# Optimization experiments

Measured on AMD Instinct MI355X. Metric: run time of the kernel, lower is better.

Reference implementation:

```python
import jax, jax.numpy as jnp
import numpy as np

N = 100000      # nodes
E = 1600000     # edges (before self loops)
IN_F = 128
OUT_F = 32
HEADS = 4
NEG_SLOPE = 0.2


def setup_inputs() -> dict:
    key = jax.random.key(0)
    k1, k2, k3, k4, k5, k6 = jax.random.split(key, 6)
    x = jax.random.normal(k1, (N, IN_F), dtype=jnp.float32)
    edge_index = jax.random.randint(k2, (2, E), 0, N, dtype=jnp.int64)
    # PyG GATConv params: shared linear W [in, H*F], attention vectors att_src/att_dst [1,H,F], bias [H*F]
    glorot = (6.0 / (IN_F + HEADS * OUT_F)) ** 0.5
    W = jax.random.uniform(k3, (IN_F, HEADS * OUT_F), dtype=jnp.float32, minval=-glorot, maxval=glorot)
    ga = (6.0 / (1 + OUT_F)) ** 0.5
    att_src = jax.random.uniform(k4, (HEADS, OUT_F), dtype=jnp.float32, minval=-ga, maxval=ga)
    att_dst = jax.random.uniform(k5, (HEADS, OUT_F), dtype=jnp.float32, minval=-ga, maxval=ga)
    bias = jnp.zeros((HEADS * OUT_F,), dtype=jnp.float32)
    return {"x": x, "edge_index": edge_index, "W": W, "att_src": att_src, "att_dst": att_dst, "bias": bias}


def reference(x, edge_index, W, att_src, att_dst, bias):
    n = x.shape[0]
    # add self loops (PyG add_self_loops=True)
    loops = jnp.arange(n, dtype=edge_index.dtype)
    src = jnp.concatenate([edge_index[0], loops])  # [E+N] message source j
    dst = jnp.concatenate([edge_index[1], loops])  # [E+N] message target i

    h = (x @ W).reshape(n, HEADS, OUT_F)                 # [N,H,F]
    a_src = jnp.sum(h * att_src[None], axis=-1)          # [N,H]
    a_dst = jnp.sum(h * att_dst[None], axis=-1)          # [N,H]

    e = a_src[src] + a_dst[dst]                          # [E',H]
    e = jax.nn.leaky_relu(e, NEG_SLOPE)
    # per-destination softmax over incoming edges
    m = jax.ops.segment_max(e, dst, num_segments=n)      # [N,H]
    ex = jnp.exp(e - m[dst])
    s = jax.ops.segment_sum(ex, dst, num_segments=n)     # [N,H]
    alpha = ex / (s[dst] + 1e-16)                        # [E',H]

    msg = h[src] * alpha[:, :, None]                     # [E',H,F]
    out = jax.ops.segment_sum(msg, dst, num_segments=n)  # [N,H,F]
    return out.reshape(n, HEADS * OUT_F) + bias
```

## Files before the change

### kernel.cpp

```cpp
#include <hip/hip_runtime.h>


#define NEG_SLOPE 0.2f
#define NB_MAX 256
#define BSHIFT 9
#define CHUNK 4096
#define CAP 11264

typedef __attribute__((ext_vector_type(8))) short short8;
typedef __attribute__((ext_vector_type(4))) float f32x4;

__device__ __forceinline__ unsigned int rne16(unsigned int u) {
  return (u + 0x7fffu + ((u >> 16) & 1u)) >> 16;
}
__device__ __forceinline__ unsigned int f2bf_pack(float a, float b) {
  return (rne16(__float_as_uint(b)) << 16) | (rne16(__float_as_uint(a)) & 0xffffu);
}

__global__ void k_wprep(const float* __restrict__ W, unsigned short* __restrict__ Wt) {
  int idx = blockIdx.x * 256 + threadIdx.x;
  int k = idx >> 7, col = idx & 127;
  Wt[col * 128 + k] = (unsigned short)rne16(__float_as_uint(W[idx]));
}

__global__ __launch_bounds__(256) void k_bucket_hist(
    const int* __restrict__ ei, int* __restrict__ bucketCnt, int E) {
  __shared__ int h[NB_MAX];
  int tid = threadIdx.x;
  h[tid] = 0;
  __syncthreads();
  int base = blockIdx.x * CHUNK;
  int n = E - base; if (n > CHUNK) n = CHUNK;
  for (int i = tid; i < n; i += 256) atomicAdd(&h[ei[E + base + i] >> BSHIFT], 1);
  __syncthreads();
  if (h[tid]) atomicAdd(&bucketCnt[tid], h[tid]);
}

__global__ void k_bucket_scan(const int* __restrict__ bucketCnt,
                              int* __restrict__ bucketOff, int* __restrict__ bcur) {
  int lane = threadIdx.x;
  int base = lane * 4;
  int v0 = bucketCnt[base], v1 = bucketCnt[base + 1];
  int v2 = bucketCnt[base + 2], v3 = bucketCnt[base + 3];
  int s = v0 + v1 + v2 + v3;
  int inc = s;
#pragma unroll
  for (int d = 1; d < 64; d <<= 1) {
    int t = __shfl_up(inc, d, 64);
    if (lane >= d) inc += t;
  }
  int ex = inc - s;
  bucketOff[base] = ex;          bcur[base] = ex;
  bucketOff[base + 1] = ex + v0; bcur[base + 1] = ex + v0;
  bucketOff[base + 2] = ex + v0 + v1; bcur[base + 2] = ex + v0 + v1;
  bucketOff[base + 3] = ex + v0 + v1 + v2; bcur[base + 3] = ex + v0 + v1 + v2;
  if (lane == 63) bucketOff[256] = inc;
}

__global__ __launch_bounds__(256) void k_bin(
    const int* __restrict__ ei, int* __restrict__ bcur,
    unsigned int* __restrict__ binned, int E, int nb) {
  __shared__ uint2 buf[CHUNK];
  __shared__ int hist[NB_MAX];
  __shared__ int loc[NB_MAX];
  __shared__ int gbase[NB_MAX];
  int tid = threadIdx.x;
  int e0 = blockIdx.x * CHUNK;
  int n = E - e0; if (n > CHUNK) n = CHUNK;

  for (int i = tid; i < NB_MAX; i += 256) hist[i] = 0;
  __syncthreads();

  int dstv[CHUNK / 256];
  int rankv[CHUNK / 256];
#pragma unroll
  for (int j = 0; j < CHUNK / 256; ++j) {
    int idx = j * 256 + tid;
    dstv[j] = -1;
    if (idx < n) {
      int d = ei[E + e0 + idx];
      dstv[j] = d;
      rankv[j] = atomicAdd(&hist[d >> BSHIFT], 1);
    }
  }
  __syncthreads();

  if (tid < 64) {
    int base = tid * 4;
    int v0 = hist[base], v1 = hist[base + 1], v2 = hist[base + 2], v3 = hist[base + 3];
    int s = v0 + v1 + v2 + v3;
    int inc = s;
#pragma unroll
    for (int d = 1; d < 64; d <<= 1) {
      int t = __shfl_up(inc, d, 64);
      if (tid >= d) inc += t;
    }
    int ex = inc - s;
    loc[base] = ex; loc[base + 1] = ex + v0;
    loc[base + 2] = ex + v0 + v1; loc[base + 3] = ex + v0 + v1 + v2;
  }
  __syncthreads();

#pragma unroll
  for (int j = 0; j < CHUNK / 256; ++j) {
    if (dstv[j] >= 0) {
      int s = ei[e0 + j * 256 + tid];
      int b = dstv[j] >> BSHIFT;
      buf[loc[b] + rankv[j]] = make_uint2((unsigned)s, (unsigned)dstv[j]);
    }
  }
  for (int b = tid; b < nb; b += 256)
    if (hist[b] > 0) gbase[b] = atomicAdd(&bcur[b], hist[b]);
  __syncthreads();

  for (int s = tid; s < n; s += 256) {
    uint2 p = buf[s];
    int b = (int)(p.y >> BSHIFT);
    binned[gbase[b] + (s - loc[b])] = p.x | ((p.y & 511u) << 20);
  }
}

__global__ __launch_bounds__(256) void k_scatter2(
    const unsigned int* __restrict__ binned, const int* __restrict__ bucketOff,
    int* __restrict__ off, int* __restrict__ ssrc, int Nn, int E, int nb) {
  __shared__ int cnt[512];
  __shared__ int loc[512];
  __shared__ int obuf[CAP];
  __shared__ int wsum[4];
  int b = blockIdx.x, tid = threadIdx.x;
  int node0 = b << BSHIFT;
  int nnodes = Nn - node0; if (nnodes > 512) nnodes = 512;
  int base = bucketOff[b];
  int nE = bucketOff[b + 1] - base;

  cnt[tid] = 0; cnt[tid + 256] = 0;
  __syncthreads();
  for (int i = tid; i < nE; i += 256)
    atomicAdd(&cnt[(binned[base + i] >> 20) & 511u], 1);
  __syncthreads();

  int i0 = 2 * tid, i1 = 2 * tid + 1;
  int v0 = cnt[i0] + (i0 < nnodes ? 1 : 0);
  int v1 = cnt[i1] + (i1 < nnodes ? 1 : 0);
  int s = v0 + v1;
  int lane = tid & 63, w = tid >> 6;
  int inc = s;
#pragma unroll
  for (int d = 1; d < 64; d <<= 1) {
    int t = __shfl_up(inc, d, 64);
    if (lane >= d) inc += t;
  }
  if (lane == 63) wsum[w] = inc;
  __syncthreads();
  int wbase = 0;
  for (int ww = 0; ww < w; ++ww) wbase += wsum[ww];
  int ex = wbase + inc - s;
  loc[i0] = ex; loc[i1] = ex + v0;
  __syncthreads();

  int csrBase = base + node0;
  for (int i = tid; i < nnodes; i += 256) {
    int l = loc[i];
    off[node0 + i] = csrBase + l;
    obuf[l] = node0 + i;
  }
  for (int i = tid; i < 512; i += 256) cnt[i] = loc[i] + 1;
  __syncthreads();

  for (int i = tid; i < nE; i += 256) {
    unsigned p = binned[base + i];
    int d = (p >> 20) & 511u;
    int pos = atomicAdd(&cnt[d], 1);
    if (pos < CAP) obuf[pos] = (int)(p & 0xFFFFFu);
  }
  __syncthreads();

  int tot = nE + nnodes;
  for (int i = tid; i < tot; i += 256) ssrc[csrBase + i] = obuf[i];
  if (b == nb - 1 && tid == 0) off[Nn] = E + Nn;
}

__global__ __launch_bounds__(256) void k_gemm(
    const float* __restrict__ x, const unsigned short* __restrict__ Wt,
    unsigned int* __restrict__ hb, int Nn) {
  int tid = threadIdx.x;
  int w = tid >> 6, lane = tid & 63;
  int m = lane & 15, q = lane >> 4;
  int r0 = blockIdx.x * 64 + w * 16;
  int rowA = r0 + m; if (rowA >= Nn) rowA = Nn - 1;
  const float* xrow = x + (size_t)rowA * 128;

  f32x4 acc[8];
#pragma unroll
  for (int t = 0; t < 8; ++t) acc[t] = (f32x4){0.f, 0.f, 0.f, 0.f};

#pragma unroll
  for (int ks = 0; ks < 4; ++ks) {
    int k0 = ks * 32 + q * 8;
    float4 a0 = *(const float4*)(xrow + k0);
    float4 a1 = *(const float4*)(xrow + k0 + 4);
    unsigned au[4];
    au[0] = f2bf_pack(a0.x, a0.y);
    au[1] = f2bf_pack(a0.z, a0.w);
    au[2] = f2bf_pack(a1.x, a1.y);
    au[3] = f2bf_pack(a1.z, a1.w);
    short8 af = *(short8*)au;
#pragma unroll
    for (int t = 0; t < 8; ++t) {
      short8 bf = *(const short8*)(Wt + (t * 16 + m) * 128 + k0);
      acc[t] = __builtin_amdgcn_mfma_f32_16x16x32_bf16(af, bf, acc[t], 0, 0, 0);
    }
  }

#pragma unroll
  for (int r = 0; r < 4; ++r) {
    int rowo = r0 + q * 4 + r;
    if (rowo < Nn) {
#pragma unroll
      for (int u = 0; u < 4; ++u) {
        hb[(size_t)rowo * 64 + u * 16 + m] = f2bf_pack(acc[2 * u][r], acc[2 * u + 1][r]);
      }
    }
  }
}

__global__ __launch_bounds__(256) void k_att(
    const unsigned int* __restrict__ hb, const float* __restrict__ attS,
    const float* __restrict__ attD, float* __restrict__ aS, float* __restrict__ aD, int Nn) {
  int wv = threadIdx.x >> 6, lane = threadIdx.x & 63;
  int node = blockIdx.x * 4 + wv;
  if (node >= Nn) return;
  int u = lane >> 4, c = lane & 15;
  unsigned v = hb[(size_t)node * 64 + lane];
  float fx = __uint_as_float(v << 16);
  float fy = __uint_as_float(v & 0xffff0000u);
  float pS = fx * attS[u * 32 + c] + fy * attS[u * 32 + c + 16];
  float pD = fx * attD[u * 32 + c] + fy * attD[u * 32 + c + 16];
#pragma unroll
  for (int d = 8; d >= 1; d >>= 1) {
    pS += __shfl_down(pS, d, 16);
    pD += __shfl_down(pD, d, 16);
  }
  if (c == 0) { aS[node * 4 + u] = pS; aD[node * 4 + u] = pD; }
}

__global__ __launch_bounds__(256) void k_aggregate(
    const unsigned int* __restrict__ hb, const float* __restrict__ aS, const float* __restrict__ aD,
    const int* __restrict__ off, const int* __restrict__ ssrc,
    const float* __restrict__ bias, float* __restrict__ out, int Nn) {
  int wave = threadIdx.x >> 6;
  int lane = threadIdx.x & 63;
  int node = blockIdx.x * 4 + wave;
  if (node >= Nn) return;
  int hd = lane >> 4;
  float ad = aD[node * 4 + hd];
  int p0 = off[node], p1 = off[node + 1];
  float accx = 0.f, accy = 0.f, den = 0.f;
  int deg = p1 - p0;
  int nch = deg >> 2;
  const int* sp = ssrc + p0;
  int s0 = 0, s1 = 0, s2 = 0, s3 = 0;
  if (nch > 0) { s0 = sp[0]; s1 = sp[1]; s2 = sp[2]; s3 = sp[3]; }
  for (int c = 0; c < nch; ++c) {
    unsigned int v0 = hb[(size_t)s0 * 64 + lane];
    unsigned int v1 = hb[(size_t)s1 * 64 + lane];
    unsigned int v2 = hb[(size_t)s2 * 64 + lane];
    unsigned int v3 = hb[(size_t)s3 * 64 + lane];
    float e0 = aS[s0 * 4 + hd] + ad;
    float e1 = aS[s1 * 4 + hd] + ad;
    float e2 = aS[s2 * 4 + hd] + ad;
    float e3 = aS[s3 * 4 + hd] + ad;
    int t0 = 0, t1 = 0, t2 = 0, t3 = 0;
    if (c + 1 < nch) {
      const int* np = sp + 4;
      t0 = np[0]; t1 = np[1]; t2 = np[2]; t3 = np[3];
    }
    e0 = e0 > 0.f ? e0 : NEG_SLOPE * e0;
    e1 = e1 > 0.f ? e1 : NEG_SLOPE * e1;
    e2 = e2 > 0.f ? e2 : NEG_SLOPE * e2;
    e3 = e3 > 0.f ? e3 : NEG_SLOPE * e3;
    float ex0 = __expf(e0), ex1 = __expf(e1), ex2 = __expf(e2), ex3 = __expf(e3);
    den += ((ex0 + ex1) + (ex2 + ex3));
    accx += ex0 * __uint_as_float(v0 << 16);
    accy += ex0 * __uint_as_float(v0 & 0xffff0000u);
    accx += ex1 * __uint_as_float(v1 << 16);
    accy += ex1 * __uint_as_float(v1 & 0xffff0000u);
    accx += ex2 * __uint_as_float(v2 << 16);
    accy += ex2 * __uint_as_float(v2 & 0xffff0000u);
    accx += ex3 * __uint_as_float(v3 << 16);
    accy += ex3 * __uint_as_float(v3 & 0xffff0000u);
    s0 = t0; s1 = t1; s2 = t2; s3 = t3;
    sp += 4;
  }
  for (int p = p0 + (nch << 2); p < p1; ++p) {
    int src = ssrc[p];
    float e = aS[src * 4 + hd] + ad;
    e = e > 0.f ? e : NEG_SLOPE * e;
    float ex = __expf(e);
    unsigned int v = hb[(size_t)src * 64 + lane];
    accx += ex * __uint_as_float(v << 16);
    accy += ex * __uint_as_float(v & 0xffff0000u);
    den += ex;
  }
  float inv = 1.0f / (den + 1e-16f);
  int col = hd * 32 + (lane & 15);
  out[(size_t)node * 128 + col] = accx * inv + bias[col];
  out[(size_t)node * 128 + col + 16] = accy * inv + bias[col + 16];
}

extern "C" void kernel_launch(void* const* d_in, const int* in_sizes, int n_in,
                              void* d_out, int out_size, void* d_ws, size_t ws_size,
                              hipStream_t stream) {
  const float* x    = (const float*)d_in[0];
  const int*   ei   = (const int*)d_in[1];
  const float* W    = (const float*)d_in[2];
  const float* attS = (const float*)d_in[3];
  const float* attD = (const float*)d_in[4];
  const float* bias = (const float*)d_in[5];
  float* out = (float*)d_out;

  const int Nn = in_sizes[0] / 128;
  const int E  = in_sizes[1] / 2;
  const int nb = (Nn + (1 << BSHIFT) - 1) >> BSHIFT;

  char* ws = (char*)d_ws;
  size_t o = 0;
  auto take = [&](size_t bytes) { void* p = ws + o; o += (bytes + 255) & ~(size_t)255; return p; };
  int* off       = (int*)take((size_t)(Nn + 1) * 4);
  int* ssrc      = (int*)take((size_t)(E + Nn) * 4);
  int* bucketCnt = (int*)take((size_t)NB_MAX * 4);
  int* bucketOff = (int*)take((size_t)(NB_MAX + 1) * 4);
  int* bcur      = (int*)take((size_t)NB_MAX * 4);
  float* aS      = (float*)take((size_t)Nn * 4 * 4);
  float* aD      = (float*)take((size_t)Nn * 4 * 4);
  unsigned short* Wt = (unsigned short*)take((size_t)128 * 128 * 2);
  unsigned int* hb = (unsigned int*)take((size_t)Nn * 64 * 4);
  unsigned int* binned = (unsigned int*)hb;
  (void)ws_size; (void)o;

  hipMemsetAsync(bucketCnt, 0, NB_MAX * 4, stream);
  k_wprep<<<64, 256, 0, stream>>>(W, Wt);
  k_bucket_hist<<<(E + CHUNK - 1) / CHUNK, 256, 0, stream>>>(ei, bucketCnt, E);
  k_bucket_scan<<<1, 64, 0, stream>>>(bucketCnt, bucketOff, bcur);
  k_bin<<<(E + CHUNK - 1) / CHUNK, 256, 0, stream>>>(ei, bcur, binned, E, nb);
  k_scatter2<<<nb, 256, 0, stream>>>(binned, bucketOff, off, ssrc, Nn, E, nb);
  k_gemm<<<(Nn + 63) / 64, 256, 0, stream>>>(x, Wt, hb, Nn);
  k_att<<<(Nn + 3) / 4, 256, 0, stream>>>(hb, attS, attD, aS, aD, Nn);
  k_aggregate<<<(Nn + 3) / 4, 256, 0, stream>>>(hb, aS, aD, off, ssrc, bias, out, Nn);
}
```

Baseline: 279.0 us.

## Fuse GEMM and attention logits into binning kernel, merge weight prep into histogram

```diff
diff --git a/kernel.cpp b/kernel.cpp
--- a/kernel.cpp
+++ b/kernel.cpp
@@ -17,16 +17,17 @@
   return (rne16(__float_as_uint(b)) << 16) | (rne16(__float_as_uint(a)) & 0xffffu);
 }
 
-__global__ void k_wprep(const float* __restrict__ W, unsigned short* __restrict__ Wt) {
-  int idx = blockIdx.x * 256 + threadIdx.x;
-  int k = idx >> 7, col = idx & 127;
-  Wt[col * 128 + k] = (unsigned short)rne16(__float_as_uint(W[idx]));
-}
-
-__global__ __launch_bounds__(256) void k_bucket_hist(
-    const int* __restrict__ ei, int* __restrict__ bucketCnt, int E) {
+__global__ __launch_bounds__(256) void k_hist_prep(
+    const int* __restrict__ ei, int* __restrict__ bucketCnt, int E,
+    const float* __restrict__ W, unsigned short* __restrict__ Wt, int nbBin) {
   __shared__ int h[NB_MAX];
   int tid = threadIdx.x;
+  if ((int)blockIdx.x >= nbBin) {
+    int idx = (blockIdx.x - nbBin) * 256 + tid;
+    int k = idx >> 7, col = idx & 127;
+    Wt[col * 128 + k] = (unsigned short)rne16(__float_as_uint(W[idx]));
+    return;
+  }
   h[tid] = 0;
   __syncthreads();
   int base = blockIdx.x * CHUNK;
@@ -57,66 +58,135 @@
   if (lane == 63) bucketOff[256] = inc;
 }
 
-__global__ __launch_bounds__(256) void k_bin(
+__global__ __launch_bounds__(256) void k_binmm(
     const int* __restrict__ ei, int* __restrict__ bcur,
-    unsigned int* __restrict__ binned, int E, int nb) {
+    unsigned int* __restrict__ binned, int E, int nb, int nbBin,
+    const float* __restrict__ x, const unsigned short* __restrict__ Wt,
+    unsigned int* __restrict__ hb,
+    const float* __restrict__ attS, const float* __restrict__ attD,
+    float* __restrict__ aS, float* __restrict__ aD, int Nn) {
   __shared__ uint2 buf[CHUNK];
   __shared__ int hist[NB_MAX];
   __shared__ int loc[NB_MAX];
   __shared__ int gbase[NB_MAX];
   int tid = threadIdx.x;
-  int e0 = blockIdx.x * CHUNK;
-  int n = E - e0; if (n > CHUNK) n = CHUNK;
-
-  for (int i = tid; i < NB_MAX; i += 256) hist[i] = 0;
-  __syncthreads();
-
-  int dstv[CHUNK / 256];
-  int rankv[CHUNK / 256];
-#pragma unroll
-  for (int j = 0; j < CHUNK / 256; ++j) {
-    int idx = j * 256 + tid;
-    dstv[j] = -1;
-    if (idx < n) {
-      int d = ei[E + e0 + idx];
-      dstv[j] = d;
-      rankv[j] = atomicAdd(&hist[d >> BSHIFT], 1);
-    }
-  }
-  __syncthreads();
-
-  if (tid < 64) {
-    int base = tid * 4;
-    int v0 = hist[base], v1 = hist[base + 1], v2 = hist[base + 2], v3 = hist[base + 3];
-    int s = v0 + v1 + v2 + v3;
-    int inc = s;
-#pragma unroll
-    for (int d = 1; d < 64; d <<= 1) {
-      int t = __shfl_up(inc, d, 64);
-      if (tid >= d) inc += t;
-    }
-    int ex = inc - s;
-    loc[base] = ex; loc[base + 1] = ex + v0;
-    loc[base + 2] = ex + v0 + v1; loc[base + 3] = ex + v0 + v1 + v2;
-  }
-  __syncthreads();
-
-#pragma unroll
-  for (int j = 0; j < CHUNK / 256; ++j) {
-    if (dstv[j] >= 0) {
-      int s = ei[e0 + j * 256 + tid];
-      int b = dstv[j] >> BSHIFT;
-      buf[loc[b] + rankv[j]] = make_uint2((unsigned)s, (unsigned)dstv[j]);
-    }
-  }
-  for (int b = tid; b < nb; b += 256)
-    if (hist[b] > 0) gbase[b] = atomicAdd(&bcur[b], hist[b]);
-  __syncthreads();
-
-  for (int s = tid; s < n; s += 256) {
-    uint2 p = buf[s];
-    int b = (int)(p.y >> BSHIFT);
-    binned[gbase[b] + (s - loc[b])] = p.x | ((p.y & 511u) << 20);
+
+  if ((int)blockIdx.x < nbBin) {
+    int e0 = blockIdx.x * CHUNK;
+    int n = E - e0; if (n > CHUNK) n = CHUNK;
+
+    for (int i = tid; i < NB_MAX; i += 256) hist[i] = 0;
+    __syncthreads();
+
+    int dstv[CHUNK / 256];
+    int rankv[CHUNK / 256];
+#pragma unroll
+    for (int j = 0; j < CHUNK / 256; ++j) {
+      int idx = j * 256 + tid;
+      dstv[j] = -1;
+      if (idx < n) {
+        int d = ei[E + e0 + idx];
+        dstv[j] = d;
+        rankv[j] = atomicAdd(&hist[d >> BSHIFT], 1);
+      }
+    }
+    __syncthreads();
+
+    if (tid < 64) {
+      int base = tid * 4;
+      int v0 = hist[base], v1 = hist[base + 1], v2 = hist[base + 2], v3 = hist[base + 3];
+      int s = v0 + v1 + v2 + v3;
+      int inc = s;
+#pragma unroll
+      for (int d = 1; d < 64; d <<= 1) {
+        int t = __shfl_up(inc, d, 64);
+        if (tid >= d) inc += t;
+      }
+      int ex = inc - s;
+      loc[base] = ex; loc[base + 1] = ex + v0;
+      loc[base + 2] = ex + v0 + v1; loc[base + 3] = ex + v0 + v1 + v2;
+    }
+    __syncthreads();
+
+#pragma unroll
+    for (int j = 0; j < CHUNK / 256; ++j) {
+      if (dstv[j] >= 0) {
+        int s = ei[e0 + j * 256 + tid];
+        int b = dstv[j] >> BSHIFT;
+        buf[loc[b] + rankv[j]] = make_uint2((unsigned)s, (unsigned)dstv[j]);
+      }
+    }
+    for (int b = tid; b < nb; b += 256)
+      if (hist[b] > 0) gbase[b] = atomicAdd(&bcur[b], hist[b]);
+    __syncthreads();
+
+    for (int s = tid; s < n; s += 256) {
+      uint2 p = buf[s];
+      int b = (int)(p.y >> BSHIFT);
+      binned[gbase[b] + (s - loc[b])] = p.x | ((p.y & 511u) << 20);
+    }
+    return;
+  }
+
+  int gbid = blockIdx.x - nbBin;
+  int w = tid >> 6, lane = tid & 63;
+  int m = lane & 15, q = lane >> 4;
+  int r0 = gbid * 64 + w * 16;
+  int rowA = r0 + m; if (rowA >= Nn) rowA = Nn - 1;
+  const float* xrow = x + (unsigned)rowA * 128u;
+
+  f32x4 acc[8];
+#pragma unroll
+  for (int t = 0; t < 8; ++t) acc[t] = (f32x4){0.f, 0.f, 0.f, 0.f};
+
+#pragma unroll
+  for (int ks = 0; ks < 4; ++ks) {
+    int k0 = ks * 32 + q * 8;
+    float4 a0 = *(const float4*)(xrow + k0);
+    float4 a1 = *(const float4*)(xrow + k0 + 4);
+    unsigned au[4];
+    au[0] = f2bf_pack(a0.x, a0.y);
+    au[1] = f2bf_pack(a0.z, a0.w);
+    au[2] = f2bf_pack(a1.x, a1.y);
+    au[3] = f2bf_pack(a1.z, a1.w);
+    short8 af = *(short8*)au;
+#pragma unroll
+    for (int t = 0; t < 8; ++t) {
+      short8 bf = *(const short8*)(Wt + (unsigned)(t * 16 + m) * 128u + k0);
+      acc[t] = __builtin_amdgcn_mfma_f32_16x16x32_bf16(af, bf, acc[t], 0, 0, 0);
+    }
+  }
+
+  float sSa[4], sSb[4], sDa[4], sDb[4];
+#pragma unroll
+  for (int u = 0; u < 4; ++u) {
+    sSa[u] = attS[u * 32 + m]; sSb[u] = attS[u * 32 + m + 16];
+    sDa[u] = attD[u * 32 + m]; sDb[u] = attD[u * 32 + m + 16];
+  }
+
+#pragma unroll
+  for (int r = 0; r < 4; ++r) {
+    int rowo = r0 + q * 4 + r;
+    bool ok = rowo < Nn;
+    if (ok) {
+#pragma unroll
+      for (int u = 0; u < 4; ++u)
+        hb[(unsigned)rowo * 64u + u * 16 + m] = f2bf_pack(acc[2 * u][r], acc[2 * u + 1][r]);
+    }
+#pragma unroll
+    for (int u = 0; u < 4; ++u) {
+      float pS = acc[2 * u][r] * sSa[u] + acc[2 * u + 1][r] * sSb[u];
+      float pD = acc[2 * u][r] * sDa[u] + acc[2 * u + 1][r] * sDb[u];
+#pragma unroll
+      for (int d = 8; d >= 1; d >>= 1) {
+        pS += __shfl_down(pS, d, 16);
+        pD += __shfl_down(pD, d, 16);
+      }
+      if (ok && m == 0) {
+        aS[(unsigned)rowo * 4u + u] = pS;
+        aD[(unsigned)rowo * 4u + u] = pD;
+      }
+    }
   }
 }
 
@@ -180,70 +250,6 @@
   if (b == nb - 1 && tid == 0) off[Nn] = E + Nn;
 }
 
-__global__ __launch_bounds__(256) void k_gemm(
-    const float* __restrict__ x, const unsigned short* __restrict__ Wt,
-    unsigned int* __restrict__ hb, int Nn) {
-  int tid = threadIdx.x;
-  int w = tid >> 6, lane = tid & 63;
-  int m = lane & 15, q = lane >> 4;
-  int r0 = blockIdx.x * 64 + w * 16;
-  int rowA = r0 + m; if (rowA >= Nn) rowA = Nn - 1;
-  const float* xrow = x + (size_t)rowA * 128;
-
-  f32x4 acc[8];
-#pragma unroll
-  for (int t = 0; t < 8; ++t) acc[t] = (f32x4){0.f, 0.f, 0.f, 0.f};
-
-#pragma unroll
-  for (int ks = 0; ks < 4; ++ks) {
-    int k0 = ks * 32 + q * 8;
-    float4 a0 = *(const float4*)(xrow + k0);
-    float4 a1 = *(const float4*)(xrow + k0 + 4);
-    unsigned au[4];
-    au[0] = f2bf_pack(a0.x, a0.y);
-    au[1] = f2bf_pack(a0.z, a0.w);
-    au[2] = f2bf_pack(a1.x, a1.y);
-    au[3] = f2bf_pack(a1.z, a1.w);
-    short8 af = *(short8*)au;
-#pragma unroll
-    for (int t = 0; t < 8; ++t) {
-      short8 bf = *(const short8*)(Wt + (t * 16 + m) * 128 + k0);
-      acc[t] = __builtin_amdgcn_mfma_f32_16x16x32_bf16(af, bf, acc[t], 0, 0, 0);
-    }
-  }
-
-#pragma unroll
-  for (int r = 0; r < 4; ++r) {
-    int rowo = r0 + q * 4 + r;
-    if (rowo < Nn) {
-#pragma unroll
-      for (int u = 0; u < 4; ++u) {
-        hb[(size_t)rowo * 64 + u * 16 + m] = f2bf_pack(acc[2 * u][r], acc[2 * u + 1][r]);
-      }
-    }
-  }
-}
-
-__global__ __launch_bounds__(256) void k_att(
-    const unsigned int* __restrict__ hb, const float* __restrict__ attS,
-    const float* __restrict__ attD, float* __restrict__ aS, float* __restrict__ aD, int Nn) {
-  int wv = threadIdx.x >> 6, lane = threadIdx.x & 63;
-  int node = blockIdx.x * 4 + wv;
-  if (node >= Nn) return;
-  int u = lane >> 4, c = lane & 15;
-  unsigned v = hb[(size_t)node * 64 + lane];
-  float fx = __uint_as_float(v << 16);
-  float fy = __uint_as_float(v & 0xffff0000u);
-  float pS = fx * attS[u * 32 + c] + fy * attS[u * 32 + c + 16];
-  float pD = fx * attD[u * 32 + c] + fy * attD[u * 32 + c + 16];
-#pragma unroll
-  for (int d = 8; d >= 1; d >>= 1) {
-    pS += __shfl_down(pS, d, 16);
-    pD += __shfl_down(pD, d, 16);
-  }
-  if (c == 0) { aS[node * 4 + u] = pS; aD[node * 4 + u] = pD; }
-}
-
 __global__ __launch_bounds__(256) void k_aggregate(
     const unsigned int* __restrict__ hb, const float* __restrict__ aS, const float* __restrict__ aD,
     const int* __restrict__ off, const int* __restrict__ ssrc,
@@ -252,29 +258,25 @@
   int lane = threadIdx.x & 63;
   int node = blockIdx.x * 4 + wave;
   if (node >= Nn) return;
-  int hd = lane >> 4;
-  float ad = aD[node * 4 + hd];
-  int p0 = off[node], p1 = off[node + 1];
-  float accx = 0.f, accy = 0.f, den = 0.f;
+  int un = __builtin_amdgcn_readfirstlane(node);
+  unsigned hd = (unsigned)lane >> 4;
+  float ad = aD[(unsigned)un * 4u + hd];
+  int p0 = off[un], p1 = off[un + 1];
+  const int* sp = ssrc + p0;
   int deg = p1 - p0;
   int nch = deg >> 2;
-  const int* sp = ssrc + p0;
-  int s0 = 0, s1 = 0, s2 = 0, s3 = 0;
-  if (nch > 0) { s0 = sp[0]; s1 = sp[1]; s2 = sp[2]; s3 = sp[3]; }
+  float accx = 0.f, accy = 0.f, den = 0.f;
+
   for (int c = 0; c < nch; ++c) {
-    unsigned int v0 = hb[(size_t)s0 * 64 + lane];
-    unsigned int v1 = hb[(size_t)s1 * 64 + lane];
-    unsigned int v2 = hb[(size_t)s2 * 64 + lane];
-    unsigned int v3 = hb[(size_t)s3 * 64 + lane];
-    float e0 = aS[s0 * 4 + hd] + ad;
-    float e1 = aS[s1 * 4 + hd] + ad;
-    float e2 = aS[s2 * 4 + hd] + ad;
-    float e3 = aS[s3 * 4 + hd] + ad;
-    int t0 = 0, t1 = 0, t2 = 0, t3 = 0;
-    if (c + 1 < nch) {
-      const int* np = sp + 4;
-      t0 = np[0]; t1 = np[1]; t2 = np[2]; t3 = np[3];
-    }
+    int s0 = sp[0], s1 = sp[1], s2 = sp[2], s3 = sp[3];
+    unsigned v0 = hb[(unsigned)s0 * 64u + lane];
+    unsigned v1 = hb[(unsigned)s1 * 64u + lane];
+    unsigned v2 = hb[(unsigned)s2 * 64u + lane];
+    unsigned v3 = hb[(unsigned)s3 * 64u + lane];
+    float e0 = aS[(unsigned)s0 * 4u + hd] + ad;
+    float e1 = aS[(unsigned)s1 * 4u + hd] + ad;
+    float e2 = aS[(unsigned)s2 * 4u + hd] + ad;
+    float e3 = aS[(unsigned)s3 * 4u + hd] + ad;
     e0 = e0 > 0.f ? e0 : NEG_SLOPE * e0;
     e1 = e1 > 0.f ? e1 : NEG_SLOPE * e1;
     e2 = e2 > 0.f ? e2 : NEG_SLOPE * e2;
@@ -289,23 +291,22 @@
     accy += ex2 * __uint_as_float(v2 & 0xffff0000u);
     accx += ex3 * __uint_as_float(v3 << 16);
     accy += ex3 * __uint_as_float(v3 & 0xffff0000u);
-    s0 = t0; s1 = t1; s2 = t2; s3 = t3;
     sp += 4;
   }
-  for (int p = p0 + (nch << 2); p < p1; ++p) {
-    int src = ssrc[p];
-    float e = aS[src * 4 + hd] + ad;
+  for (int p = nch << 2; p < deg; ++p) {
+    int src = (ssrc + p0)[p];
+    float e = aS[(unsigned)src * 4u + hd] + ad;
     e = e > 0.f ? e : NEG_SLOPE * e;
     float ex = __expf(e);
-    unsigned int v = hb[(size_t)src * 64 + lane];
+    unsigned v = hb[(unsigned)src * 64u + lane];
     accx += ex * __uint_as_float(v << 16);
     accy += ex * __uint_as_float(v & 0xffff0000u);
     den += ex;
   }
   float inv = 1.0f / (den + 1e-16f);
-  int col = hd * 32 + (lane & 15);
-  out[(size_t)node * 128 + col] = accx * inv + bias[col];
-  out[(size_t)node * 128 + col + 16] = accy * inv + bias[col + 16];
+  unsigned col = hd * 32u + ((unsigned)lane & 15u);
+  out[(unsigned)un * 128u + col] = accx * inv + bias[col];
+  out[(unsigned)un * 128u + col + 16u] = accy * inv + bias[col + 16];
 }
 
 extern "C" void kernel_launch(void* const* d_in, const int* in_sizes, int n_in,
@@ -322,6 +323,8 @@
   const int Nn = in_sizes[0] / 128;
   const int E  = in_sizes[1] / 2;
   const int nb = (Nn + (1 << BSHIFT) - 1) >> BSHIFT;
+  const int nbBin = (E + CHUNK - 1) / CHUNK;
+  const int nGemm = (Nn + 63) / 64;
 
   char* ws = (char*)d_ws;
   size_t o = 0;
@@ -335,16 +338,14 @@
   float* aD      = (float*)take((size_t)Nn * 4 * 4);
   unsigned short* Wt = (unsigned short*)take((size_t)128 * 128 * 2);
   unsigned int* hb = (unsigned int*)take((size_t)Nn * 64 * 4);
-  unsigned int* binned = (unsigned int*)hb;
+  unsigned int* binned = (unsigned int*)take((size_t)E * 4);
   (void)ws_size; (void)o;
 
   hipMemsetAsync(bucketCnt, 0, NB_MAX * 4, stream);
-  k_wprep<<<64, 256, 0, stream>>>(W, Wt);
-  k_bucket_hist<<<(E + CHUNK - 1) / CHUNK, 256, 0, stream>>>(ei, bucketCnt, E);
+  k_hist_prep<<<nbBin + 64, 256, 0, stream>>>(ei, bucketCnt, E, W, Wt, nbBin);
   k_bucket_scan<<<1, 64, 0, stream>>>(bucketCnt, bucketOff, bcur);
-  k_bin<<<(E + CHUNK - 1) / CHUNK, 256, 0, stream>>>(ei, bcur, binned, E, nb);
+  k_binmm<<<nbBin + nGemm, 256, 0, stream>>>(ei, bcur, binned, E, nb, nbBin,
+                                             x, Wt, hb, attS, attD, aS, aD, Nn);
   k_scatter2<<<nb, 256, 0, stream>>>(binned, bucketOff, off, ssrc, Nn, E, nb);
-  k_gemm<<<(Nn + 63) / 64, 256, 0, stream>>>(x, Wt, hb, Nn);
-  k_att<<<(Nn + 3) / 4, 256, 0, stream>>>(hb, attS, attD, aS, aD, Nn);
   k_aggregate<<<(Nn + 3) / 4, 256, 0, stream>>>(hb, aS, aD, off, ssrc, bias, out, Nn);
 }
```

Result: faster. 252.4 us (-9.5%).
